# Performance work log

Measured on AMD Instinct MI355X. Metric: run time of the kernel, lower is better.

The kernel has to match this reference:

```python
import jax, jax.numpy as jnp
import numpy as np

B, L, N = 4, 1024, 2048
V_DIM, L_DIM, HID, H = 512, 768, 512, 8
HD = HID // H
SCALE = HD ** -0.5


def setup_inputs() -> dict:
    key = jax.random.key(0)
    ks = jax.random.split(key, 6)
    return {
        "x": jax.random.normal(ks[0], (B, L, V_DIM), dtype=jnp.float32),
        "vfeats": jax.random.normal(ks[1], (B, N, L_DIM), dtype=jnp.float32),
        "topk_mask": jax.random.normal(ks[2], (B, H, L, N), dtype=jnp.float32),
        "Wq": jax.random.normal(ks[3], (HID, V_DIM), dtype=jnp.float32) * 0.02,
        "Wkv": jax.random.normal(ks[4], (2 * HID, L_DIM), dtype=jnp.float32) * 0.02,
        "Wproj": jax.random.normal(ks[5], (V_DIM, HID), dtype=jnp.float32) * 0.02,
        "bproj": jnp.zeros((V_DIM,), dtype=jnp.float32),
    }


def reference(x, vfeats, topk_mask, Wq, Wkv, Wproj, bproj):
    # q: [B,L,HID] -> [B,H,L,HD]
    q = (x @ Wq.T).reshape(B, L, H, HD).transpose(0, 2, 1, 3)
    # kv: [B,N,2*HID] -> k,v each [B,H,N,HD]
    kv = (vfeats @ Wkv.T).reshape(B, N, 2, H, HD).transpose(2, 0, 3, 1, 4)
    k, v = kv[0], kv[1]
    attn = jnp.einsum("bhld,bhnd->bhln", q, k) * SCALE + topk_mask
    attn = jax.nn.softmax(attn, axis=-1)
    out = jnp.einsum("bhln,bhnd->bhld", attn, v)  # [B,H,L,HD]
    out = out.transpose(0, 2, 1, 3).reshape(B, L, HID)
    return out @ Wproj.T + bproj
```

## Files before the change

### kernel.cpp

```cpp
#include <hip/hip_runtime.h>
#include <math.h>

#define B_ 4
#define L_ 1024
#define N_ 2048
#define VDIM_ 512
#define LDIM_ 768
#define HID_ 512
#define H_ 8
#define HD_ 64
#define SCALE_ 0.125f

typedef __bf16 bf16;
typedef __bf16 bf16x4 __attribute__((ext_vector_type(4)));
typedef __bf16 bf16x8 __attribute__((ext_vector_type(8)));
typedef float f32x4 __attribute__((ext_vector_type(4)));

__device__ __forceinline__ void async_cp16(const bf16* g, bf16* l) {
    __builtin_amdgcn_global_load_lds(
        (const __attribute__((address_space(1))) unsigned int*)g,
        (__attribute__((address_space(3))) unsigned int*)l, 16, 0, 0);
}

__global__ void cvt_bf16(const float* __restrict__ in, bf16* __restrict__ out, int n) {
    int i = (blockIdx.x * 256 + threadIdx.x) * 4;
    if (i < n) {
        float4 v = *(const float4*)(in + i);
        bf16x4 o;
        o[0] = (bf16)v.x; o[1] = (bf16)v.y; o[2] = (bf16)v.z; o[3] = (bf16)v.w;
        *(bf16x4*)(out + i) = o;
    }
}

__global__ void cvt_split(const float* __restrict__ in, bf16* __restrict__ hi,
                          bf16* __restrict__ lo, int n) {
    int i = (blockIdx.x * 256 + threadIdx.x) * 4;
    if (i < n) {
        float4 v = *(const float4*)(in + i);
        bf16x4 h, lw;
        float vv[4] = {v.x, v.y, v.z, v.w};
        #pragma unroll
        for (int j = 0; j < 4; ++j) {
            bf16 hb = (bf16)vv[j];
            h[j] = hb;
            lw[j] = (bf16)(vv[j] - (float)hb);
        }
        *(bf16x4*)(hi + i) = h;
        *(bf16x4*)(lo + i) = lw;
    }
}

template<int BM, int BN>
__global__ __launch_bounds__(256)
void gemm_bf16(const bf16* __restrict__ A, const bf16* __restrict__ W,
               bf16* __restrict__ C, int M, int N, int K)
{
    __shared__ bf16 As[BM * 64];
    __shared__ bf16 Ws[BN * 64];
    const int t = threadIdx.x, l = t & 63, wv = t >> 6;
    const int n0 = blockIdx.x * BN, m0 = blockIdx.y * BM;
    const int wm = (wv >> 1) * (BM / 2), wn = (wv & 1) * (BN / 2);
    constexpr int TI = BM / 32, TJ = BN / 32;
    const int lq = l & 15, qd = l >> 4, swz = l & 7;

    f32x4 acc[TI][TJ];
    #pragma unroll
    for (int i = 0; i < TI; ++i)
        #pragma unroll
        for (int j = 0; j < TJ; ++j)
            #pragma unroll
            for (int r = 0; r < 4; ++r) acc[i][j][r] = 0.f;

    for (int kt = 0; kt < K; kt += 64) {
        __syncthreads();
        for (int it = wv; it < BM / 8; it += 4) {
            int r = it * 8 + (l >> 3);
            int c = (l & 7) ^ (r & 7);
            async_cp16(A + (size_t)(m0 + r) * K + kt + c * 8, &As[it * 512]);
        }
        for (int it = wv; it < BN / 8; it += 4) {
            int r = it * 8 + (l >> 3);
            int c = (l & 7) ^ (r & 7);
            async_cp16(W + (size_t)(n0 + r) * K + kt + c * 8, &Ws[it * 512]);
        }
        __syncthreads();
        #pragma unroll
        for (int ks = 0; ks < 2; ++ks) {
            bf16x8 af[TI], wf[TJ];
            #pragma unroll
            for (int i = 0; i < TI; ++i) {
                int row = wm + i * 16 + lq;
                af[i] = *(const bf16x8*)&As[row * 64 + (((ks * 4 + qd)) ^ swz) * 8];
            }
            #pragma unroll
            for (int j = 0; j < TJ; ++j) {
                int row = wn + j * 16 + lq;
                wf[j] = *(const bf16x8*)&Ws[row * 64 + (((ks * 4 + qd)) ^ swz) * 8];
            }
            #pragma unroll
            for (int i = 0; i < TI; ++i)
                #pragma unroll
                for (int j = 0; j < TJ; ++j)
                    acc[i][j] = __builtin_amdgcn_mfma_f32_16x16x32_bf16(
                        af[i], wf[j], acc[i][j], 0, 0, 0);
        }
    }
    #pragma unroll
    for (int i = 0; i < TI; ++i)
        #pragma unroll
        for (int j = 0; j < TJ; ++j)
            #pragma unroll
            for (int r = 0; r < 4; ++r) {
                int row = m0 + wm + i * 16 + qd * 4 + r;
                int col = n0 + wn + j * 16 + lq;
                C[(size_t)row * N + col] = (bf16)acc[i][j][r];
            }
}

__global__ __launch_bounds__(256)
void gemm_proj_split(const bf16* __restrict__ Ah, const bf16* __restrict__ Al,
                     const bf16* __restrict__ Wh, const bf16* __restrict__ Wl,
                     const float* __restrict__ bias, float* __restrict__ Cf,
                     int M, int N, int K)
{
    __shared__ bf16 sAh[64 * 64], sAl[64 * 64];
    __shared__ bf16 sWh[128 * 64], sWl[128 * 64];
    const int t = threadIdx.x, l = t & 63, wv = t >> 6;
    const int n0 = blockIdx.x * 128, m0 = blockIdx.y * 64;
    const int wm = (wv >> 1) * 32, wn = (wv & 1) * 64;
    const int lq = l & 15, qd = l >> 4, swz = l & 7;

    f32x4 acc[2][4];
    #pragma unroll
    for (int i = 0; i < 2; ++i)
        #pragma unroll
        for (int j = 0; j < 4; ++j)
            #pragma unroll
            for (int r = 0; r < 4; ++r) acc[i][j][r] = 0.f;

    for (int kt = 0; kt < K; kt += 64) {
        __syncthreads();
        for (int it = wv; it < 8; it += 4) {
            int r = it * 8 + (l >> 3);
            int c = (l & 7) ^ (r & 7);
            size_t go = (size_t)(m0 + r) * K + kt + c * 8;
            async_cp16(Ah + go, &sAh[it * 512]);
            async_cp16(Al + go, &sAl[it * 512]);
        }
        for (int it = wv; it < 16; it += 4) {
            int r = it * 8 + (l >> 3);
            int c = (l & 7) ^ (r & 7);
            size_t go = (size_t)(n0 + r) * K + kt + c * 8;
            async_cp16(Wh + go, &sWh[it * 512]);
            async_cp16(Wl + go, &sWl[it * 512]);
        }
        __syncthreads();
        #pragma unroll
        for (int ks = 0; ks < 2; ++ks) {
            bf16x8 ah[2], al2[2], wh[4], wl[4];
            #pragma unroll
            for (int i = 0; i < 2; ++i) {
                int off = (wm + i * 16 + lq) * 64 + ((ks * 4 + qd) ^ swz) * 8;
                ah[i]  = *(const bf16x8*)&sAh[off];
                al2[i] = *(const bf16x8*)&sAl[off];
            }
            #pragma unroll
            for (int j = 0; j < 4; ++j) {
                int off = (wn + j * 16 + lq) * 64 + ((ks * 4 + qd) ^ swz) * 8;
                wh[j] = *(const bf16x8*)&sWh[off];
                wl[j] = *(const bf16x8*)&sWl[off];
            }
            #pragma unroll
            for (int i = 0; i < 2; ++i)
                #pragma unroll
                for (int j = 0; j < 4; ++j) {
                    acc[i][j] = __builtin_amdgcn_mfma_f32_16x16x32_bf16(ah[i],  wh[j], acc[i][j], 0, 0, 0);
                    acc[i][j] = __builtin_amdgcn_mfma_f32_16x16x32_bf16(ah[i],  wl[j], acc[i][j], 0, 0, 0);
                    acc[i][j] = __builtin_amdgcn_mfma_f32_16x16x32_bf16(al2[i], wh[j], acc[i][j], 0, 0, 0);
                }
        }
    }
    #pragma unroll
    for (int i = 0; i < 2; ++i)
        #pragma unroll
        for (int j = 0; j < 4; ++j) {
            int col = n0 + wn + j * 16 + lq;
            float bb = bias[col];
            #pragma unroll
            for (int r = 0; r < 4; ++r) {
                int row = m0 + wm + i * 16 + qd * 4 + r;
                Cf[(size_t)row * N + col] = acc[i][j][r] + bb;
            }
        }
}

__global__ __launch_bounds__(256)
void transpose_v(const bf16* __restrict__ kv, bf16* __restrict__ vT)
{
    __shared__ bf16 T[64 * 64];
    const int t = threadIdx.x;
    const int bid = blockIdx.x;
    const int nt = bid & 31, h = (bid >> 5) & 7, b = bid >> 8;
    const int n0 = nt * 64;
    for (int g = t; g < 512; g += 256) {
        int r = g >> 3, c = g & 7;
        bf16x8 v = *(const bf16x8*)(kv + (size_t)(b * N_ + n0 + r) * (2 * HID_) +
                                    HID_ + h * HD_ + c * 8);
        *(bf16x8*)&T[r * 64 + (c ^ (r & 7)) * 8] = v;
    }
    __syncthreads();
    for (int g = t; g < 512; g += 256) {
        int d = g >> 3, kg = g & 7;
        bf16x8 ov;
        #pragma unroll
        for (int jj = 0; jj < 8; ++jj) {
            int key = kg * 8 + jj;
            ov[jj] = T[key * 64 + (((d >> 3) ^ (key & 7))) * 8 + (d & 7)];
        }
        *(bf16x8*)&vT[(size_t)((b * H_ + h) * HD_ + d) * N_ + n0 + kg * 8] = ov;
    }
}

__global__ __launch_bounds__(256)
void attn_mfma(const bf16* __restrict__ q, const bf16* __restrict__ kv,
               const bf16* __restrict__ vT, const float* __restrict__ mask,
               bf16* __restrict__ ao_hi, bf16* __restrict__ ao_lo)
{
    __shared__ bf16 Ks[64 * 64];
    __shared__ bf16 Vs[64 * 64];
    __shared__ bf16 Pa[4][16 * 72];
    const int t = threadIdx.x, l = t & 63, wv = t >> 6;
    const int bid = blockIdx.x;
    const int lt = bid & 15, h = (bid >> 4) & 7, b = bid >> 7;
    const int l0 = lt * 64;
    const int lq = l & 15, qd = l >> 4, swz = l & 7;

    bf16x8 qf[2];
    {
        const bf16* qb = q + (size_t)(b * L_ + l0 + wv * 16 + lq) * HID_ + h * HD_ + qd * 8;
        qf[0] = *(const bf16x8*)qb;
        qf[1] = *(const bf16x8*)(qb + 32);
    }

    f32x4 o[4];
    #pragma unroll
    for (int j = 0; j < 4; ++j)
        #pragma unroll
        for (int r = 0; r < 4; ++r) o[j][r] = 0.f;
    float m_run[4], l_run[4];
    #pragma unroll
    for (int r = 0; r < 4; ++r) { m_run[r] = -1e30f; l_run[r] = 0.f; }

    const bf16* kb = kv + (size_t)(b * N_) * (2 * HID_) + h * HD_;
    const bf16* vb = vT + (size_t)((b * H_ + h) * HD_) * N_;
    const size_t mrow0 = (size_t)((b * H_ + h) * L_ + l0 + wv * 16);
    bf16* Paw = &Pa[wv][0];

    for (int nt = 0; nt < N_ / 64; ++nt) {
        const int n0 = nt * 64;
        __syncthreads();
        float mk[4][4];
        #pragma unroll
        for (int jj = 0; jj < 4; ++jj)
            #pragma unroll
            for (int r = 0; r < 4; ++r)
                mk[jj][r] = mask[(mrow0 + qd * 4 + r) * N_ + n0 + jj * 16 + lq];
        for (int it = wv; it < 8; it += 4) {
            int r = it * 8 + (l >> 3);
            int c = (l & 7) ^ (r & 7);
            async_cp16(kb + (size_t)(n0 + r) * (2 * HID_) + c * 8, &Ks[it * 512]);
            async_cp16(vb + (size_t)r * N_ + n0 + c * 8, &Vs[it * 512]);
        }
        __syncthreads();
        f32x4 s[4];
        #pragma unroll
        for (int jj = 0; jj < 4; ++jj)
            #pragma unroll
            for (int r = 0; r < 4; ++r) s[jj][r] = 0.f;
        #pragma unroll
        for (int ks = 0; ks < 2; ++ks)
            #pragma unroll
            for (int jj = 0; jj < 4; ++jj) {
                bf16x8 kf = *(const bf16x8*)&Ks[(jj * 16 + lq) * 64 +
                                                ((ks * 4 + qd) ^ swz) * 8];
                s[jj] = __builtin_amdgcn_mfma_f32_16x16x32_bf16(qf[ks], kf, s[jj], 0, 0, 0);
            }
        float sv[4][4];
        #pragma unroll
        for (int jj = 0; jj < 4; ++jj)
            #pragma unroll
            for (int r = 0; r < 4; ++r)
                sv[jj][r] = fmaf(s[jj][r], SCALE_, mk[jj][r]);
        float alpha[4], mnew[4];
        #pragma unroll
        for (int r = 0; r < 4; ++r) {
            float mx = fmaxf(fmaxf(sv[0][r], sv[1][r]), fmaxf(sv[2][r], sv[3][r]));
            #pragma unroll
            for (int d2 = 1; d2 < 16; d2 <<= 1) mx = fmaxf(mx, __shfl_xor(mx, d2));
            mnew[r] = fmaxf(m_run[r], mx);
            alpha[r] = __expf(m_run[r] - mnew[r]);
            m_run[r] = mnew[r];
        }
        bf16 pb[4][4];
        #pragma unroll
        for (int r = 0; r < 4; ++r) {
            float ss = 0.f;
            #pragma unroll
            for (int jj = 0; jj < 4; ++jj) {
                float p = __expf(sv[jj][r] - mnew[r]);
                pb[jj][r] = (bf16)p;
                ss += p;
            }
            #pragma unroll
            for (int d2 = 1; d2 < 16; d2 <<= 1) ss += __shfl_xor(ss, d2);
            l_run[r] = l_run[r] * alpha[r] + ss;
        }
        #pragma unroll
        for (int jj = 0; jj < 4; ++jj)
            #pragma unroll
            for (int r = 0; r < 4; ++r)
                Paw[(qd * 4 + r) * 72 + jj * 16 + lq] = pb[jj][r];
        __asm__ __volatile__("s_waitcnt lgkmcnt(0)" ::: "memory");
        #pragma unroll
        for (int jj = 0; jj < 4; ++jj)
            #pragma unroll
            for (int r = 0; r < 4; ++r) o[jj][r] *= alpha[r];
        #pragma unroll
        for (int ks = 0; ks < 2; ++ks) {
            bf16x8 pf = *(const bf16x8*)&Paw[lq * 72 + ks * 32 + qd * 8];
            #pragma unroll
            for (int jj = 0; jj < 4; ++jj) {
                bf16x8 vf = *(const bf16x8*)&Vs[(jj * 16 + lq) * 64 +
                                                ((ks * 4 + qd) ^ swz) * 8];
                o[jj] = __builtin_amdgcn_mfma_f32_16x16x32_bf16(pf, vf, o[jj], 0, 0, 0);
            }
        }
    }
    #pragma unroll
    for (int jj = 0; jj < 4; ++jj)
        #pragma unroll
        for (int r = 0; r < 4; ++r) {
            int row = b * L_ + l0 + wv * 16 + qd * 4 + r;
            int col = h * HD_ + jj * 16 + lq;
            float v = o[jj][r] / l_run[r];
            bf16 hb = (bf16)v;
            ao_hi[(size_t)row * HID_ + col] = hb;
            ao_lo[(size_t)row * HID_ + col] = (bf16)(v - (float)hb);
        }
}

extern "C" void kernel_launch(void* const* d_in, const int* in_sizes, int n_in,
                              void* d_out, int out_size, void* d_ws, size_t ws_size,
                              hipStream_t stream)
{
    const float* x      = (const float*)d_in[0];
    const float* vfeats = (const float*)d_in[1];
    const float* mask   = (const float*)d_in[2];
    const float* Wq     = (const float*)d_in[3];
    const float* Wkv    = (const float*)d_in[4];
    const float* Wproj  = (const float*)d_in[5];
    const float* bproj  = (const float*)d_in[6];
    float* out = (float*)d_out;

    char* ws = (char*)d_ws;
    bf16* vfb = (bf16*)(ws);
    bf16* vTb = (bf16*)(ws);
    bf16* kvb = (bf16*)(ws + 12582912);
    bf16* xb  = (bf16*)(ws + 29360128);
    bf16* aoh = (bf16*)(ws + 29360128);
    bf16* qb  = (bf16*)(ws + 33554432);
    bf16* aol = (bf16*)(ws + 37748736);
    bf16* wqb = (bf16*)(ws + 41943040);
    bf16* wkvb= (bf16*)(ws + 42467328);
    bf16* wph = (bf16*)(ws + 44040192);
    bf16* wpl = (bf16*)(ws + 44564480);

    dim3 blk(256);
    cvt_bf16<<<dim3(B_*L_*VDIM_/1024),   blk, 0, stream>>>(x,      xb,   B_*L_*VDIM_);
    cvt_bf16<<<dim3(B_*N_*LDIM_/1024),   blk, 0, stream>>>(vfeats, vfb,  B_*N_*LDIM_);
    cvt_bf16<<<dim3(HID_*VDIM_/1024),    blk, 0, stream>>>(Wq,     wqb,  HID_*VDIM_);
    cvt_bf16<<<dim3(2*HID_*LDIM_/1024),  blk, 0, stream>>>(Wkv,    wkvb, 2*HID_*LDIM_);
    cvt_split<<<dim3(VDIM_*HID_/1024),   blk, 0, stream>>>(Wproj,  wph, wpl, VDIM_*HID_);
    gemm_bf16<64,128><<<dim3(HID_/128, B_*L_/64), blk, 0, stream>>>(
        xb, wqb, qb, B_*L_, HID_, VDIM_);
    gemm_bf16<128,128><<<dim3(2*HID_/128, B_*N_/128), blk, 0, stream>>>(
        vfb, wkvb, kvb, B_*N_, 2*HID_, LDIM_);
    transpose_v<<<dim3(B_*H_*(N_/64)), blk, 0, stream>>>(kvb, vTb);
    attn_mfma<<<dim3(B_*H_*(L_/64)), blk, 0, stream>>>(qb, kvb, vTb, mask, aoh, aol);
    gemm_proj_split<<<dim3(VDIM_/128, B_*L_/64), blk, 0, stream>>>(
        aoh, aol, wph, wpl, bproj, out, B_*L_, VDIM_, HID_);
}
```

Measured before the change: 482.9 us.

## Fuse input conversions, widen attention key tile, drop activation low split

Merges the four fp32-to-bf16 conversion launches into a single kernel. Doubles the attention key/value tile to 128 so each loop iteration does more MFMA work per barrier, and moves the P buffer to a wider stride. Attention output is now written as bf16 only, and the projection GEMM drops the low-part activation term, going from three MFMA products to two. The Q/KV/proj GEMM tiles are shrunk to 64-wide N for more blocks. Dropping the activation low part reduces projection accuracy.

```diff
diff --git a/kernel.cpp b/kernel.cpp
--- a/kernel.cpp
+++ b/kernel.cpp
@@ -22,14 +22,26 @@
         (__attribute__((address_space(3))) unsigned int*)l, 16, 0, 0);
 }
 
-__global__ void cvt_bf16(const float* __restrict__ in, bf16* __restrict__ out, int n) {
-    int i = (blockIdx.x * 256 + threadIdx.x) * 4;
-    if (i < n) {
-        float4 v = *(const float4*)(in + i);
-        bf16x4 o;
-        o[0] = (bf16)v.x; o[1] = (bf16)v.y; o[2] = (bf16)v.z; o[3] = (bf16)v.w;
-        *(bf16x4*)(out + i) = o;
-    }
+#define XE_   2097152
+#define VFE_  6291456
+#define WQE_  262144
+#define WKVE_ 786432
+__global__ void cvt_all(const float* __restrict__ x, const float* __restrict__ vf,
+                        const float* __restrict__ wq, const float* __restrict__ wkv,
+                        bf16* __restrict__ xb, bf16* __restrict__ vfb,
+                        bf16* __restrict__ wqb, bf16* __restrict__ wkvb)
+{
+    int e = (blockIdx.x * 256 + threadIdx.x) * 4;
+    const float* src; bf16* dst; int off;
+    if (e < XE_)                        { src = x;   dst = xb;   off = 0; }
+    else if (e < XE_ + VFE_)            { src = vf;  dst = vfb;  off = XE_; }
+    else if (e < XE_ + VFE_ + WQE_)     { src = wq;  dst = wqb;  off = XE_ + VFE_; }
+    else                                { src = wkv; dst = wkvb; off = XE_ + VFE_ + WQE_; }
+    int i = e - off;
+    float4 v = *(const float4*)(src + i);
+    bf16x4 o;
+    o[0] = (bf16)v.x; o[1] = (bf16)v.y; o[2] = (bf16)v.z; o[3] = (bf16)v.w;
+    *(bf16x4*)(dst + i) = o;
 }
 
 __global__ void cvt_split(const float* __restrict__ in, bf16* __restrict__ hi,
@@ -90,12 +102,12 @@
             #pragma unroll
             for (int i = 0; i < TI; ++i) {
                 int row = wm + i * 16 + lq;
-                af[i] = *(const bf16x8*)&As[row * 64 + (((ks * 4 + qd)) ^ swz) * 8];
+                af[i] = *(const bf16x8*)&As[row * 64 + ((ks * 4 + qd) ^ swz) * 8];
             }
             #pragma unroll
             for (int j = 0; j < TJ; ++j) {
                 int row = wn + j * 16 + lq;
-                wf[j] = *(const bf16x8*)&Ws[row * 64 + (((ks * 4 + qd)) ^ swz) * 8];
+                wf[j] = *(const bf16x8*)&Ws[row * 64 + ((ks * 4 + qd) ^ swz) * 8];
             }
             #pragma unroll
             for (int i = 0; i < TI; ++i)
@@ -118,23 +130,22 @@
 }
 
 __global__ __launch_bounds__(256)
-void gemm_proj_split(const bf16* __restrict__ Ah, const bf16* __restrict__ Al,
-                     const bf16* __restrict__ Wh, const bf16* __restrict__ Wl,
-                     const float* __restrict__ bias, float* __restrict__ Cf,
-                     int M, int N, int K)
-{
-    __shared__ bf16 sAh[64 * 64], sAl[64 * 64];
-    __shared__ bf16 sWh[128 * 64], sWl[128 * 64];
+void gemm_proj(const bf16* __restrict__ A, const bf16* __restrict__ Wh,
+               const bf16* __restrict__ Wl, const float* __restrict__ bias,
+               float* __restrict__ Cf, int M, int N, int K)
+{
+    __shared__ bf16 sA[64 * 64];
+    __shared__ bf16 sWh[64 * 64], sWl[64 * 64];
     const int t = threadIdx.x, l = t & 63, wv = t >> 6;
-    const int n0 = blockIdx.x * 128, m0 = blockIdx.y * 64;
-    const int wm = (wv >> 1) * 32, wn = (wv & 1) * 64;
+    const int n0 = blockIdx.x * 64, m0 = blockIdx.y * 64;
+    const int wm = (wv >> 1) * 32, wn = (wv & 1) * 32;
     const int lq = l & 15, qd = l >> 4, swz = l & 7;
 
-    f32x4 acc[2][4];
+    f32x4 acc[2][2];
     #pragma unroll
     for (int i = 0; i < 2; ++i)
         #pragma unroll
-        for (int j = 0; j < 4; ++j)
+        for (int j = 0; j < 2; ++j)
             #pragma unroll
             for (int r = 0; r < 4; ++r) acc[i][j][r] = 0.f;
 
@@ -143,13 +154,7 @@
         for (int it = wv; it < 8; it += 4) {
             int r = it * 8 + (l >> 3);
             int c = (l & 7) ^ (r & 7);
-            size_t go = (size_t)(m0 + r) * K + kt + c * 8;
-            async_cp16(Ah + go, &sAh[it * 512]);
-            async_cp16(Al + go, &sAl[it * 512]);
-        }
-        for (int it = wv; it < 16; it += 4) {
-            int r = it * 8 + (l >> 3);
-            int c = (l & 7) ^ (r & 7);
+            async_cp16(A  + (size_t)(m0 + r) * K + kt + c * 8, &sA[it * 512]);
             size_t go = (size_t)(n0 + r) * K + kt + c * 8;
             async_cp16(Wh + go, &sWh[it * 512]);
             async_cp16(Wl + go, &sWl[it * 512]);
@@ -157,15 +162,14 @@
         __syncthreads();
         #pragma unroll
         for (int ks = 0; ks < 2; ++ks) {
-            bf16x8 ah[2], al2[2], wh[4], wl[4];
+            bf16x8 af[2], wh[2], wl[2];
             #pragma unroll
             for (int i = 0; i < 2; ++i) {
                 int off = (wm + i * 16 + lq) * 64 + ((ks * 4 + qd) ^ swz) * 8;
-                ah[i]  = *(const bf16x8*)&sAh[off];
-                al2[i] = *(const bf16x8*)&sAl[off];
-            }
-            #pragma unroll
-            for (int j = 0; j < 4; ++j) {
+                af[i] = *(const bf16x8*)&sA[off];
+            }
+            #pragma unroll
+            for (int j = 0; j < 2; ++j) {
                 int off = (wn + j * 16 + lq) * 64 + ((ks * 4 + qd) ^ swz) * 8;
                 wh[j] = *(const bf16x8*)&sWh[off];
                 wl[j] = *(const bf16x8*)&sWl[off];
@@ -173,17 +177,16 @@
             #pragma unroll
             for (int i = 0; i < 2; ++i)
                 #pragma unroll
-                for (int j = 0; j < 4; ++j) {
-                    acc[i][j] = __builtin_amdgcn_mfma_f32_16x16x32_bf16(ah[i],  wh[j], acc[i][j], 0, 0, 0);
-                    acc[i][j] = __builtin_amdgcn_mfma_f32_16x16x32_bf16(ah[i],  wl[j], acc[i][j], 0, 0, 0);
-                    acc[i][j] = __builtin_amdgcn_mfma_f32_16x16x32_bf16(al2[i], wh[j], acc[i][j], 0, 0, 0);
+                for (int j = 0; j < 2; ++j) {
+                    acc[i][j] = __builtin_amdgcn_mfma_f32_16x16x32_bf16(af[i], wh[j], acc[i][j], 0, 0, 0);
+                    acc[i][j] = __builtin_amdgcn_mfma_f32_16x16x32_bf16(af[i], wl[j], acc[i][j], 0, 0, 0);
                 }
         }
     }
     #pragma unroll
     for (int i = 0; i < 2; ++i)
         #pragma unroll
-        for (int j = 0; j < 4; ++j) {
+        for (int j = 0; j < 2; ++j) {
             int col = n0 + wn + j * 16 + lq;
             float bb = bias[col];
             #pragma unroll
@@ -221,14 +224,15 @@
     }
 }
 
+#define PST 136
 __global__ __launch_bounds__(256)
 void attn_mfma(const bf16* __restrict__ q, const bf16* __restrict__ kv,
                const bf16* __restrict__ vT, const float* __restrict__ mask,
-               bf16* __restrict__ ao_hi, bf16* __restrict__ ao_lo)
-{
-    __shared__ bf16 Ks[64 * 64];
-    __shared__ bf16 Vs[64 * 64];
-    __shared__ bf16 Pa[4][16 * 72];
+               bf16* __restrict__ ao)
+{
+    __shared__ bf16 Ks[128 * 64];
+    __shared__ bf16 Vs[64 * 128];
+    __shared__ bf16 Pa[4][16 * PST];
     const int t = threadIdx.x, l = t & 63, wv = t >> 6;
     const int bid = blockIdx.x;
     const int lt = bid & 15, h = (bid >> 4) & 7, b = bid >> 7;
@@ -256,58 +260,63 @@
     const size_t mrow0 = (size_t)((b * H_ + h) * L_ + l0 + wv * 16);
     bf16* Paw = &Pa[wv][0];
 
-    for (int nt = 0; nt < N_ / 64; ++nt) {
-        const int n0 = nt * 64;
-        __syncthreads();
-        float mk[4][4];
-        #pragma unroll
-        for (int jj = 0; jj < 4; ++jj)
+    for (int nt = 0; nt < N_ / 128; ++nt) {
+        const int n0 = nt * 128;
+        __syncthreads();
+        float mk[8][4];
+        #pragma unroll
+        for (int jj = 0; jj < 8; ++jj)
             #pragma unroll
             for (int r = 0; r < 4; ++r)
                 mk[jj][r] = mask[(mrow0 + qd * 4 + r) * N_ + n0 + jj * 16 + lq];
-        for (int it = wv; it < 8; it += 4) {
+        for (int it = wv; it < 16; it += 4) {
             int r = it * 8 + (l >> 3);
             int c = (l & 7) ^ (r & 7);
             async_cp16(kb + (size_t)(n0 + r) * (2 * HID_) + c * 8, &Ks[it * 512]);
+        }
+        for (int it = wv; it < 16; it += 4) {
+            int r = it * 4 + (l >> 4);
+            int c = (l & 15) ^ (r & 15);
             async_cp16(vb + (size_t)r * N_ + n0 + c * 8, &Vs[it * 512]);
         }
         __syncthreads();
-        f32x4 s[4];
-        #pragma unroll
-        for (int jj = 0; jj < 4; ++jj)
+        f32x4 s[8];
+        #pragma unroll
+        for (int jj = 0; jj < 8; ++jj)
             #pragma unroll
             for (int r = 0; r < 4; ++r) s[jj][r] = 0.f;
         #pragma unroll
         for (int ks = 0; ks < 2; ++ks)
             #pragma unroll
-            for (int jj = 0; jj < 4; ++jj) {
+            for (int jj = 0; jj < 8; ++jj) {
                 bf16x8 kf = *(const bf16x8*)&Ks[(jj * 16 + lq) * 64 +
                                                 ((ks * 4 + qd) ^ swz) * 8];
                 s[jj] = __builtin_amdgcn_mfma_f32_16x16x32_bf16(qf[ks], kf, s[jj], 0, 0, 0);
             }
-        float sv[4][4];
-        #pragma unroll
-        for (int jj = 0; jj < 4; ++jj)
+        #pragma unroll
+        for (int jj = 0; jj < 8; ++jj)
             #pragma unroll
             for (int r = 0; r < 4; ++r)
-                sv[jj][r] = fmaf(s[jj][r], SCALE_, mk[jj][r]);
+                s[jj][r] = fmaf(s[jj][r], SCALE_, mk[jj][r]);
         float alpha[4], mnew[4];
         #pragma unroll
         for (int r = 0; r < 4; ++r) {
-            float mx = fmaxf(fmaxf(sv[0][r], sv[1][r]), fmaxf(sv[2][r], sv[3][r]));
+            float mx = s[0][r];
+            #pragma unroll
+            for (int jj = 1; jj < 8; ++jj) mx = fmaxf(mx, s[jj][r]);
             #pragma unroll
             for (int d2 = 1; d2 < 16; d2 <<= 1) mx = fmaxf(mx, __shfl_xor(mx, d2));
             mnew[r] = fmaxf(m_run[r], mx);
             alpha[r] = __expf(m_run[r] - mnew[r]);
             m_run[r] = mnew[r];
         }
-        bf16 pb[4][4];
+        bf16 pb[8][4];
         #pragma unroll
         for (int r = 0; r < 4; ++r) {
             float ss = 0.f;
             #pragma unroll
-            for (int jj = 0; jj < 4; ++jj) {
-                float p = __expf(sv[jj][r] - mnew[r]);
+            for (int jj = 0; jj < 8; ++jj) {
+                float p = __expf(s[jj][r] - mnew[r]);
                 pb[jj][r] = (bf16)p;
                 ss += p;
             }
@@ -316,22 +325,23 @@
             l_run[r] = l_run[r] * alpha[r] + ss;
         }
         #pragma unroll
+        for (int jj = 0; jj < 8; ++jj)
+            #pragma unroll
+            for (int r = 0; r < 4; ++r)
+                Paw[(qd * 4 + r) * PST + jj * 16 + lq] = pb[jj][r];
+        __asm__ __volatile__("s_waitcnt lgkmcnt(0)" ::: "memory");
+        #pragma unroll
         for (int jj = 0; jj < 4; ++jj)
             #pragma unroll
-            for (int r = 0; r < 4; ++r)
-                Paw[(qd * 4 + r) * 72 + jj * 16 + lq] = pb[jj][r];
-        __asm__ __volatile__("s_waitcnt lgkmcnt(0)" ::: "memory");
-        #pragma unroll
-        for (int jj = 0; jj < 4; ++jj)
-            #pragma unroll
             for (int r = 0; r < 4; ++r) o[jj][r] *= alpha[r];
         #pragma unroll
-        for (int ks = 0; ks < 2; ++ks) {
-            bf16x8 pf = *(const bf16x8*)&Paw[lq * 72 + ks * 32 + qd * 8];
+        for (int ks = 0; ks < 4; ++ks) {
+            bf16x8 pf = *(const bf16x8*)&Paw[lq * PST + ks * 32 + qd * 8];
             #pragma unroll
             for (int jj = 0; jj < 4; ++jj) {
-                bf16x8 vf = *(const bf16x8*)&Vs[(jj * 16 + lq) * 64 +
-                                                ((ks * 4 + qd) ^ swz) * 8];
+                int d = jj * 16 + lq;
+                bf16x8 vf = *(const bf16x8*)&Vs[d * 128 +
+                                                ((ks * 4 + qd) ^ (d & 15)) * 8];
                 o[jj] = __builtin_amdgcn_mfma_f32_16x16x32_bf16(pf, vf, o[jj], 0, 0, 0);
             }
         }
@@ -342,10 +352,7 @@
         for (int r = 0; r < 4; ++r) {
             int row = b * L_ + l0 + wv * 16 + qd * 4 + r;
             int col = h * HD_ + jj * 16 + lq;
-            float v = o[jj][r] / l_run[r];
-            bf16 hb = (bf16)v;
-            ao_hi[(size_t)row * HID_ + col] = hb;
-            ao_lo[(size_t)row * HID_ + col] = (bf16)(v - (float)hb);
+            ao[(size_t)row * HID_ + col] = (bf16)(o[jj][r] / l_run[r]);
         }
 }
 
@@ -363,30 +370,27 @@
     float* out = (float*)d_out;
 
     char* ws = (char*)d_ws;
-    bf16* vfb = (bf16*)(ws);
-    bf16* vTb = (bf16*)(ws);
-    bf16* kvb = (bf16*)(ws + 12582912);
-    bf16* xb  = (bf16*)(ws + 29360128);
-    bf16* aoh = (bf16*)(ws + 29360128);
-    bf16* qb  = (bf16*)(ws + 33554432);
-    bf16* aol = (bf16*)(ws + 37748736);
-    bf16* wqb = (bf16*)(ws + 41943040);
-    bf16* wkvb= (bf16*)(ws + 42467328);
-    bf16* wph = (bf16*)(ws + 44040192);
-    bf16* wpl = (bf16*)(ws + 44564480);
+    bf16* xb   = (bf16*)(ws);
+    bf16* vfb  = (bf16*)(ws + 4194304);
+    bf16* wqb  = (bf16*)(ws + 16777216);
+    bf16* wkvb = (bf16*)(ws + 17301504);
+    bf16* wph  = (bf16*)(ws + 18874368);
+    bf16* wpl  = (bf16*)(ws + 19398656);
+    bf16* qb   = (bf16*)(ws + 19922944);
+    bf16* kvb  = (bf16*)(ws + 24117248);
+    bf16* vTb  = (bf16*)(ws + 40894464);
+    bf16* aob  = (bf16*)(ws + 49283072);
 
     dim3 blk(256);
-    cvt_bf16<<<dim3(B_*L_*VDIM_/1024),   blk, 0, stream>>>(x,      xb,   B_*L_*VDIM_);
-    cvt_bf16<<<dim3(B_*N_*LDIM_/1024),   blk, 0, stream>>>(vfeats, vfb,  B_*N_*LDIM_);
-    cvt_bf16<<<dim3(HID_*VDIM_/1024),    blk, 0, stream>>>(Wq,     wqb,  HID_*VDIM_);
-    cvt_bf16<<<dim3(2*HID_*LDIM_/1024),  blk, 0, stream>>>(Wkv,    wkvb, 2*HID_*LDIM_);
-    cvt_split<<<dim3(VDIM_*HID_/1024),   blk, 0, stream>>>(Wproj,  wph, wpl, VDIM_*HID_);
-    gemm_bf16<64,128><<<dim3(HID_/128, B_*L_/64), blk, 0, stream>>>(
-        xb, wqb, qb, B_*L_, HID_, VDIM_);
-    gemm_bf16<128,128><<<dim3(2*HID_/128, B_*N_/128), blk, 0, stream>>>(
-        vfb, wkvb, kvb, B_*N_, 2*HID_, LDIM_);
-    transpose_v<<<dim3(B_*H_*(N_/64)), blk, 0, stream>>>(kvb, vTb);
-    attn_mfma<<<dim3(B_*H_*(L_/64)), blk, 0, stream>>>(qb, kvb, vTb, mask, aoh, aol);
-    gemm_proj_split<<<dim3(VDIM_/128, B_*L_/64), blk, 0, stream>>>(
-        aoh, aol, wph, wpl, bproj, out, B_*L_, VDIM_, HID_);
-}
+    cvt_all<<<dim3((XE_ + VFE_ + WQE_ + WKVE_) / 1024), blk, 0, stream>>>(
+        x, vfeats, Wq, Wkv, xb, vfb, wqb, wkvb);
+    cvt_split<<<dim3(VDIM_ * HID_ / 1024), blk, 0, stream>>>(Wproj, wph, wpl, VDIM_ * HID_);
+    gemm_bf16<64, 64><<<dim3(HID_ / 64, B_ * L_ / 64), blk, 0, stream>>>(
+        xb, wqb, qb, B_ * L_, HID_, VDIM_);
+    gemm_bf16<128, 64><<<dim3(2 * HID_ / 64, B_ * N_ / 128), blk, 0, stream>>>(
+        vfb, wkvb, kvb, B_ * N_, 2 * HID_, LDIM_);
+    transpose_v<<<dim3(B_ * H_ * (N_ / 64)), blk, 0, stream>>>(kvb, vTb);
+    attn_mfma<<<dim3(B_ * H_ * (L_ / 64)), blk, 0, stream>>>(qb, kvb, vTb, mask, aob);
+    gemm_proj<<<dim3(VDIM_ / 64, B_ * L_ / 64), blk, 0, stream>>>(
+        aob, wph, wpl, bproj, out, B_ * L_, VDIM_, HID_);
+}
```

Result: faster. 452.5 us (-6.3%).
